# Kernel optimization log

Hardware: AMD Instinct MI355X
Metric: run time of the kernel (lower is better)

The kernel has to match this reference:

```python
import jax, jax.numpy as jnp
import numpy as np

EPS = 1e-8
BETA = 0.02          # bisector-band sharpness
ALPHA_UNION = 8.0    # exp-union strength
W_MIN, W_MAX = 0.005, 0.5
RAW_TEMP = 5.0       # width squash temperature
REL_TEMP = 0.05      # seed-relevance softmax temperature
A_MIN, A_MAX = 0.5, 2.0  # anisotropy eigenvalue range


def setup_inputs() -> dict:
    key = jax.random.key(0)
    k1, k2, k3, k4, k5 = jax.random.split(key, 5)
    N, S = 65536, 32
    return {
        "points_uv": jax.random.uniform(k1, (N, 2), dtype=jnp.float32),
        "seeds_raw": jax.random.uniform(k2, (S, 2), dtype=jnp.float32),
        "w_raw": jax.random.normal(k3, (1,), dtype=jnp.float32),
        "theta": jax.random.normal(k4, (S,), dtype=jnp.float32),
        "a_raw": jax.random.normal(k5, (S,), dtype=jnp.float32),
    }


def _metric_matrices(theta, a_raw):
    # anisotropic 2x2 SPD metrics M_s = R^T diag(a, 1/a) R
    t = jnp.tanh(a_raw)
    a = 0.5 * (A_MAX - A_MIN) * t + 0.5 * (A_MAX + A_MIN)  # (S,)
    c, s = jnp.cos(theta), jnp.sin(theta)
    R = jnp.stack([jnp.stack([c, -s], -1), jnp.stack([s, c], -1)], -2)  # (S,2,2)
    dvec = jnp.stack([a, 1.0 / (a + EPS)], -1)  # (S,2)
    return jnp.einsum("ska,sk,skb->sab", R, dvec, R)  # (S,2,2)


def reference(points_uv, seeds_raw, w_raw, theta, a_raw):
    S = seeds_raw.shape[0]
    # half-thickness around the Voronoi bisector
    w = W_MIN + (W_MAX - W_MIN) * jax.nn.sigmoid(w_raw[0] / RAW_TEMP)
    M = _metric_matrices(theta, a_raw)  # (S,2,2)

    # point-to-seed diffs with periodic wrapping on both u and v
    diff = points_uv[:, None, :] - seeds_raw[None, :, :]  # (N,S,2)
    diff = diff - jnp.round(diff)

    # anisotropic distances d_i(x) = sqrt(diff^T M_i diff)
    d = jnp.sqrt(jnp.einsum("nsa,sab,nsb->ns", diff, M, diff) + EPS)  # (N,S)

    # soft seed relevance -> soft pair weights P_ij (upper triangular, normalized)
    w_soft = jax.nn.softmax(-d / REL_TEMP, axis=1)  # (N,S)
    pair = w_soft[:, :, None] * w_soft[:, None, :]  # (N,S,S)
    mask = jnp.triu(jnp.ones((S, S), dtype=points_uv.dtype), k=1)
    pair = pair * mask
    P = pair / (pair.sum(axis=(1, 2), keepdims=True) + EPS)

    # bisector band: B_ij = sigmoid((w - |d_i - d_j|_smooth) / beta)
    Delta = d[:, :, None] - d[:, None, :]  # (N,S,S)
    abs_smooth = jnp.sqrt(Delta * Delta + EPS)
    B = jax.nn.sigmoid((w - abs_smooth) / BETA)

    # union over i<j pairs: rho = 1 - exp(-alpha * sum S_ij)
    S_sum = jnp.sum(P * B, axis=(1, 2))  # (N,)
    rho = 1.0 - jnp.exp(-ALPHA_UNION * S_sum)
    return rho
```

## Files before the change

kernel.cpp:

```cpp
#include <hip/hip_runtime.h>
#include <math.h>


#define LOG2E  1.4426950408889634f
#define EPSF   1e-8f
#define TAB_D  8192.0f
#define TAB_N  8320
#define BLOCK  512
#define PPB    64

__device__ __forceinline__ float tabB(const float* tab, unsigned a, unsigned b) {
    const unsigned hi = a > b ? a : b;
    const unsigned lo = a > b ? b : a;
    return *(const float*)((const char*)tab + (hi - lo));
}

__global__ __launch_bounds__(BLOCK) void voronoi_tab(
    const float* __restrict__ points,
    const float* __restrict__ seeds,
    const float* __restrict__ w_raw,
    const float* __restrict__ theta,
    const float* __restrict__ a_raw,
    float* __restrict__ out,
    int N, int nTiles)
{
    __shared__ float    s_tab[TAB_N];
    __shared__ unsigned s_di[PPB * 32];
    __shared__ float    s_w [PPB * 32];
    __shared__ float    s_su[32], s_sv[32], s_m00[32], s_m01[32], s_m11[32];

    const int t = threadIdx.x;

    const float wr = w_raw[0];
    const float sg = __builtin_amdgcn_rcpf(1.0f + exp2f(wr * (-LOG2E / 5.0f)));
    const float w  = 0.005f + 0.495f * sg;

    if (t < 32) {
        const float x  = a_raw[t];
        const float z  = exp2f(2.0f * LOG2E * x);
        const float th = (z - 1.0f) * __builtin_amdgcn_rcpf(z + 1.0f);
        const float a  = 0.75f * th + 1.25f;
        const float ia = __builtin_amdgcn_rcpf(a + EPSF);
        const float cs = __cosf(theta[t]);
        const float sn = __sinf(theta[t]);
        const float S2 = TAB_D * TAB_D;
        s_m00[t] = (a * cs * cs + ia * sn * sn) * S2;
        s_m01[t] = (cs * sn * (ia - a)) * S2;
        s_m11[t] = (a * sn * sn + ia * cs * cs) * S2;
        s_su[t]  = seeds[2 * t];
        s_sv[t]  = seeds[2 * t + 1];
    }

    {
        const float kC = (LOG2E / 0.02f) / TAB_D;
        const float kB = -w * (LOG2E / 0.02f);
        for (int k = t; k < TAB_N; k += BLOCK) {
            const float y = exp2f(fmaf((float)k, kC, kB));
            s_tab[k] = __builtin_amdgcn_rcpf(1.0f + y);
        }
    }
    __syncthreads();

    const int pb = t >> 3;
    const int g  = t & 7;
    const int s0 = g * 4;

    const float4 su4  = *(const float4*)&s_su[s0];
    const float4 sv4  = *(const float4*)&s_sv[s0];
    const float4 m004 = *(const float4*)&s_m00[s0];
    const float4 m014 = *(const float4*)&s_m01[s0];
    const float4 m114 = *(const float4*)&s_m11[s0];

    unsigned* dbase = &s_di[pb * 32];
    float*    wbase = &s_w [pb * 32];

    const float EPS_Q = 1e-8f * TAB_D * TAB_D;
    const float cE    = -(20.0f * LOG2E) / TAB_D;

    for (int tile = blockIdx.x; tile < nTiles; tile += gridDim.x) {
        const int p = tile * PPB + pb;
        if (p < N) {
            const float2 uv = ((const float2*)points)[p];
            const float u = uv.x, v = uv.y;

            float4 d4;
#define DIST(SU, SV, M00, M01, M11, OUTD)                                    \
            {                                                                \
                float du = u - (SU); du -= rintf(du);                        \
                float dv = v - (SV); dv -= rintf(dv);                        \
                float q = fmaf(du * du, (M00),                               \
                          fmaf(2.0f * du * dv, (M01),                       \
                          fmaf(dv * dv, (M11), EPS_Q)));                     \
                (OUTD) = sqrtf(q);                                           \
            }
            DIST(su4.x, sv4.x, m004.x, m014.x, m114.x, d4.x)
            DIST(su4.y, sv4.y, m004.y, m014.y, m114.y, d4.y)
            DIST(su4.z, sv4.z, m004.z, m014.z, m114.z, d4.z)
            DIST(su4.w, sv4.w, m004.w, m014.w, m114.w, d4.w)

            float4 e4;
            e4.x = exp2f(d4.x * cE);
            e4.y = exp2f(d4.y * cE);
            e4.z = exp2f(d4.z * cE);
            e4.w = exp2f(d4.w * cE);
            float Z = (e4.x + e4.y) + (e4.z + e4.w);
            Z += __shfl_xor(Z, 1, 64);
            Z += __shfl_xor(Z, 2, 64);
            Z += __shfl_xor(Z, 4, 64);
            const float rcpZ = __builtin_amdgcn_rcpf(Z);
            float4 w4;
            w4.x = e4.x * rcpZ; w4.y = e4.y * rcpZ;
            w4.z = e4.z * rcpZ; w4.w = e4.w * rcpZ;
            float sumsq = w4.x * w4.x;
            sumsq = fmaf(w4.y, w4.y, sumsq);
            sumsq = fmaf(w4.z, w4.z, sumsq);
            sumsq = fmaf(w4.w, w4.w, sumsq);

            uint4 ii;
            ii.x = ((unsigned)(d4.x + 0.5f)) << 2;
            ii.y = ((unsigned)(d4.y + 0.5f)) << 2;
            ii.z = ((unsigned)(d4.z + 0.5f)) << 2;
            ii.w = ((unsigned)(d4.w + 0.5f)) << 2;

            *(uint4*) (dbase + s0) = ii;
            *(float4*)(wbase + s0) = w4;

            float accb = 0.0f;
            {
                float b0 = tabB(s_tab, ii.x, ii.y) * w4.y;
                b0 = fmaf(tabB(s_tab, ii.x, ii.z), w4.z, b0);
                b0 = fmaf(tabB(s_tab, ii.x, ii.w), w4.w, b0);
                float b1 = tabB(s_tab, ii.y, ii.z) * w4.z;
                b1 = fmaf(tabB(s_tab, ii.y, ii.w), w4.w, b1);
                float b2 = tabB(s_tab, ii.z, ii.w) * w4.w;
                accb = fmaf(w4.x, b0, accb);
                accb = fmaf(w4.y, b1, accb);
                accb = fmaf(w4.z, b2, accb);
            }

#define ROT(R, ACC)                                                          \
            {                                                                \
                const int gj = ((g + (R)) & 7) * 4;                          \
                const uint4  ij = *(const uint4*) (dbase + gj);              \
                const float4 wj = *(const float4*)(wbase + gj);              \
                float b0, b1, b2, b3;                                        \
                b0 =      tabB(s_tab, ii.x, ij.x) * wj.x;                    \
                b0 = fmaf(tabB(s_tab, ii.x, ij.y), wj.y, b0);                \
                b0 = fmaf(tabB(s_tab, ii.x, ij.z), wj.z, b0);                \
                b0 = fmaf(tabB(s_tab, ii.x, ij.w), wj.w, b0);                \
                b1 =      tabB(s_tab, ii.y, ij.x) * wj.x;                    \
                b1 = fmaf(tabB(s_tab, ii.y, ij.y), wj.y, b1);                \
                b1 = fmaf(tabB(s_tab, ii.y, ij.z), wj.z, b1);                \
                b1 = fmaf(tabB(s_tab, ii.y, ij.w), wj.w, b1);                \
                b2 =      tabB(s_tab, ii.z, ij.x) * wj.x;                    \
                b2 = fmaf(tabB(s_tab, ii.z, ij.y), wj.y, b2);                \
                b2 = fmaf(tabB(s_tab, ii.z, ij.z), wj.z, b2);                \
                b2 = fmaf(tabB(s_tab, ii.z, ij.w), wj.w, b2);                \
                b3 =      tabB(s_tab, ii.w, ij.x) * wj.x;                    \
                b3 = fmaf(tabB(s_tab, ii.w, ij.y), wj.y, b3);                \
                b3 = fmaf(tabB(s_tab, ii.w, ij.z), wj.z, b3);                \
                b3 = fmaf(tabB(s_tab, ii.w, ij.w), wj.w, b3);                \
                (ACC) = fmaf(w4.x, b0, (ACC));                               \
                (ACC) = fmaf(w4.y, b1, (ACC));                               \
                (ACC) = fmaf(w4.z, b2, (ACC));                               \
                (ACC) = fmaf(w4.w, b3, (ACC));                               \
            }

            ROT(1, accb)
            ROT(2, accb)
            ROT(3, accb)
            float acc4 = 0.0f;
            ROT(4, acc4)
            accb = fmaf(0.5f, acc4, accb);

            float nb = accb, sq = sumsq;
            nb += __shfl_xor(nb, 1, 64);  sq += __shfl_xor(sq, 1, 64);
            nb += __shfl_xor(nb, 2, 64);  sq += __shfl_xor(sq, 2, 64);
            nb += __shfl_xor(nb, 4, 64);  sq += __shfl_xor(sq, 4, 64);

            const float den   = fmaxf(0.5f * (1.0f - sq), 0.0f) + EPSF;
            const float ratio = nb * __builtin_amdgcn_rcpf(den);
            const float rho   = 1.0f - exp2f(ratio * (-8.0f * LOG2E));
            if (g == 0) out[p] = rho;
        }
    }
}

extern "C" void kernel_launch(void* const* d_in, const int* in_sizes, int n_in,
                              void* d_out, int out_size, void* d_ws, size_t ws_size,
                              hipStream_t stream) {
    const float* points = (const float*)d_in[0];
    const float* seeds  = (const float*)d_in[1];
    const float* w_raw  = (const float*)d_in[2];
    const float* theta  = (const float*)d_in[3];
    const float* a_raw  = (const float*)d_in[4];
    float* out = (float*)d_out;

    const int N = in_sizes[0] / 2;
    const int nTiles = (N + PPB - 1) / PPB;
    const int grid = nTiles < 768 ? nTiles : 768;

    voronoi_tab<<<grid, BLOCK, 0, stream>>>(points, seeds, w_raw, theta, a_raw,
                                            out, N, nTiles);
}
```

Baseline: 17.57 us.

## Compute cross-group bisector sigmoids directly and shrink the signed lookup table

The 4x4 cross-group pair terms now compute the bisector sigmoid directly with exp2 and a reciprocal instead of gathering from a shared-memory table with data-dependent indices. The remaining intra-group pairs use a smaller signed-difference table with clamped indices. The persistent grid-stride loop is replaced by one 32-point tile per 256-thread block, with a higher occupancy hint. This trades scattered LDS gathers and their bank conflicts for transcendental ALU work. Every block now rebuilds its own smaller table, and there are many more blocks doing so.

```diff
diff --git a/kernel.cpp b/kernel.cpp
--- a/kernel.cpp
+++ b/kernel.cpp
@@ -4,30 +4,26 @@
 
 #define LOG2E  1.4426950408889634f
 #define EPSF   1e-8f
-#define TAB_D  8192.0f
-#define TAB_N  8320
-#define BLOCK  512
-#define PPB    64
+#define TSCALE 2048.0f
+#define TAB_N  2048
+#define TMIDB  4096
+#define BLOCK  256
+#define PPB    32
+#define SSTR   40
 
-__device__ __forceinline__ float tabB(const float* tab, unsigned a, unsigned b) {
-    const unsigned hi = a > b ? a : b;
-    const unsigned lo = a > b ? b : a;
-    return *(const float*)((const char*)tab + (hi - lo));
-}
-
-__global__ __launch_bounds__(BLOCK) void voronoi_tab(
+__global__ __launch_bounds__(BLOCK, 8) void voronoi_v4(
     const float* __restrict__ points,
     const float* __restrict__ seeds,
     const float* __restrict__ w_raw,
     const float* __restrict__ theta,
     const float* __restrict__ a_raw,
     float* __restrict__ out,
-    int N, int nTiles)
+    int N)
 {
-    __shared__ float    s_tab[TAB_N];
-    __shared__ unsigned s_di[PPB * 32];
-    __shared__ float    s_w [PPB * 32];
-    __shared__ float    s_su[32], s_sv[32], s_m00[32], s_m01[32], s_m11[32];
+    __shared__ float s_tab[TAB_N];
+    __shared__ float s_dd[PPB * SSTR];
+    __shared__ float s_ww[PPB * SSTR];
+    __shared__ float s_su[32], s_sv[32], s_m00[32], s_m01[32], s_m11[32];
 
     const int t = threadIdx.x;
 
@@ -43,19 +39,19 @@
         const float ia = __builtin_amdgcn_rcpf(a + EPSF);
         const float cs = __cosf(theta[t]);
         const float sn = __sinf(theta[t]);
-        const float S2 = TAB_D * TAB_D;
+        const float S2 = TSCALE * TSCALE;
         s_m00[t] = (a * cs * cs + ia * sn * sn) * S2;
-        s_m01[t] = (cs * sn * (ia - a)) * S2;
+        s_m01[t] = (2.0f * cs * sn * (ia - a)) * S2;
         s_m11[t] = (a * sn * sn + ia * cs * cs) * S2;
         s_su[t]  = seeds[2 * t];
         s_sv[t]  = seeds[2 * t + 1];
     }
-
     {
-        const float kC = (LOG2E / 0.02f) / TAB_D;
-        const float kB = -w * (LOG2E / 0.02f);
+        const float kC = (50.0f * LOG2E) / TSCALE;
+        const float kB = -w * (50.0f * LOG2E);
         for (int k = t; k < TAB_N; k += BLOCK) {
-            const float y = exp2f(fmaf((float)k, kC, kB));
+            const float ad = fabsf((float)(k - 1024));
+            const float y  = exp2f(fmaf(ad, kC, kB));
             s_tab[k] = __builtin_amdgcn_rcpf(1.0f + y);
         }
     }
@@ -64,6 +60,8 @@
     const int pb = t >> 3;
     const int g  = t & 7;
     const int s0 = g * 4;
+    const int p  = blockIdx.x * PPB + pb;
+    if (p >= N) return;
 
     const float4 su4  = *(const float4*)&s_su[s0];
     const float4 sv4  = *(const float4*)&s_sv[s0];
@@ -71,119 +69,114 @@
     const float4 m014 = *(const float4*)&s_m01[s0];
     const float4 m114 = *(const float4*)&s_m11[s0];
 
-    unsigned* dbase = &s_di[pb * 32];
-    float*    wbase = &s_w [pb * 32];
+    const float2 uv = ((const float2*)points)[p];
+    const float u = uv.x, v = uv.y;
 
-    const float EPS_Q = 1e-8f * TAB_D * TAB_D;
-    const float cE    = -(20.0f * LOG2E) / TAB_D;
+    const float EPS_Q = 1e-8f * TSCALE * TSCALE;
+    float4 d4;
+#define DIST(SU, SV, M00, M01, M11, OUTD)                                  \
+    {                                                                      \
+        float du = u - (SU); du -= rintf(du);                              \
+        float dv = v - (SV); dv -= rintf(dv);                              \
+        float q = fmaf(du * du, (M00),                                     \
+                  fmaf(du * dv, (M01),                                     \
+                  fmaf(dv * dv, (M11), EPS_Q)));                           \
+        (OUTD) = sqrtf(q);                                                 \
+    }
+    DIST(su4.x, sv4.x, m004.x, m014.x, m114.x, d4.x)
+    DIST(su4.y, sv4.y, m004.y, m014.y, m114.y, d4.y)
+    DIST(su4.z, sv4.z, m004.z, m014.z, m114.z, d4.z)
+    DIST(su4.w, sv4.w, m004.w, m014.w, m114.w, d4.w)
 
-    for (int tile = blockIdx.x; tile < nTiles; tile += gridDim.x) {
-        const int p = tile * PPB + pb;
-        if (p < N) {
-            const float2 uv = ((const float2*)points)[p];
-            const float u = uv.x, v = uv.y;
+    const float cE = -(20.0f * LOG2E) / TSCALE;
+    float4 e4;
+    e4.x = exp2f(d4.x * cE);
+    e4.y = exp2f(d4.y * cE);
+    e4.z = exp2f(d4.z * cE);
+    e4.w = exp2f(d4.w * cE);
+    float Z = (e4.x + e4.y) + (e4.z + e4.w);
+    Z += __shfl_xor(Z, 1, 64);
+    Z += __shfl_xor(Z, 2, 64);
+    Z += __shfl_xor(Z, 4, 64);
+    const float rcpZ = __builtin_amdgcn_rcpf(Z);
+    float4 w4;
+    w4.x = e4.x * rcpZ; w4.y = e4.y * rcpZ;
+    w4.z = e4.z * rcpZ; w4.w = e4.w * rcpZ;
+    float sumsq = w4.x * w4.x;
+    sumsq = fmaf(w4.y, w4.y, sumsq);
+    sumsq = fmaf(w4.z, w4.z, sumsq);
+    sumsq = fmaf(w4.w, w4.w, sumsq);
 
-            float4 d4;
-#define DIST(SU, SV, M00, M01, M11, OUTD)                                    \
-            {                                                                \
-                float du = u - (SU); du -= rintf(du);                        \
-                float dv = v - (SV); dv -= rintf(dv);                        \
-                float q = fmaf(du * du, (M00),                               \
-                          fmaf(2.0f * du * dv, (M01),                       \
-                          fmaf(dv * dv, (M11), EPS_Q)));                     \
-                (OUTD) = sqrtf(q);                                           \
-            }
-            DIST(su4.x, sv4.x, m004.x, m014.x, m114.x, d4.x)
-            DIST(su4.y, sv4.y, m004.y, m014.y, m114.y, d4.y)
-            DIST(su4.z, sv4.z, m004.z, m014.z, m114.z, d4.z)
-            DIST(su4.w, sv4.w, m004.w, m014.w, m114.w, d4.w)
+    float* db = &s_dd[pb * SSTR];
+    float* wb = &s_ww[pb * SSTR];
+    *(float4*)(db + s0) = d4;
+    *(float4*)(wb + s0) = w4;
 
-            float4 e4;
-            e4.x = exp2f(d4.x * cE);
-            e4.y = exp2f(d4.y * cE);
-            e4.z = exp2f(d4.z * cE);
-            e4.w = exp2f(d4.w * cE);
-            float Z = (e4.x + e4.y) + (e4.z + e4.w);
-            Z += __shfl_xor(Z, 1, 64);
-            Z += __shfl_xor(Z, 2, 64);
-            Z += __shfl_xor(Z, 4, 64);
-            const float rcpZ = __builtin_amdgcn_rcpf(Z);
-            float4 w4;
-            w4.x = e4.x * rcpZ; w4.y = e4.y * rcpZ;
-            w4.z = e4.z * rcpZ; w4.w = e4.w * rcpZ;
-            float sumsq = w4.x * w4.x;
-            sumsq = fmaf(w4.y, w4.y, sumsq);
-            sumsq = fmaf(w4.z, w4.z, sumsq);
-            sumsq = fmaf(w4.w, w4.w, sumsq);
+    const char* tb = (const char*)s_tab;
+    int K = (int)(TSCALE * w) + 370;
+    if (K > 1023) K = 1023;
+    const int lo = TMIDB - 4 * K, hi = TMIDB + 4 * K;
+#define TBODY(DI, DJ, WJ, ACC)                                             \
+    {                                                                      \
+        int off = (int)fmaf((DI) - (DJ), 4.0f, (float)(TMIDB + 2));        \
+        off = off < lo ? lo : (off > hi ? hi : off);                       \
+        off &= ~3;                                                         \
+        const float B = *(const float*)(tb + off);                         \
+        (ACC) = fmaf((WJ), B, (ACC));                                      \
+    }
+    float b0, b1, b2, b3;
+    b0 = 0.0f; b1 = 0.0f; b2 = 0.0f; b3 = 0.0f;
+    TBODY(d4.x, d4.y, w4.y, b0)
+    TBODY(d4.x, d4.z, w4.z, b0)
+    TBODY(d4.x, d4.w, w4.w, b0)
+    TBODY(d4.y, d4.z, w4.z, b1)
+    TBODY(d4.y, d4.w, w4.w, b1)
+    TBODY(d4.z, d4.w, w4.w, b2)
 
-            uint4 ii;
-            ii.x = ((unsigned)(d4.x + 0.5f)) << 2;
-            ii.y = ((unsigned)(d4.y + 0.5f)) << 2;
-            ii.z = ((unsigned)(d4.z + 0.5f)) << 2;
-            ii.w = ((unsigned)(d4.w + 0.5f)) << 2;
+    const float C1 = (50.0f * LOG2E) / TSCALE;
+    const float C0 = -w * (50.0f * LOG2E);
+#define EBODY(DI, DJ, WJ, ACC)                                             \
+    {                                                                      \
+        const float ex = exp2f(fmaf(fabsf((DI) - (DJ)), C1, C0));          \
+        const float B  = __builtin_amdgcn_rcpf(1.0f + ex);                 \
+        (ACC) = fmaf((WJ), B, (ACC));                                      \
+    }
+#define ROTE(R, HALF)                                                      \
+    {                                                                      \
+        const int gj = ((g + (R)) & 7) * 4;                                \
+        const float4 dj = *(const float4*)(db + gj);                       \
+        float4 wj = *(const float4*)(wb + gj);                             \
+        if (HALF) {                                                        \
+            wj.x *= 0.5f; wj.y *= 0.5f; wj.z *= 0.5f; wj.w *= 0.5f;        \
+        }                                                                  \
+        EBODY(d4.x, dj.x, wj.x, b0) EBODY(d4.x, dj.y, wj.y, b0)            \
+        EBODY(d4.x, dj.z, wj.z, b0) EBODY(d4.x, dj.w, wj.w, b0)            \
+        EBODY(d4.y, dj.x, wj.x, b1) EBODY(d4.y, dj.y, wj.y, b1)            \
+        EBODY(d4.y, dj.z, wj.z, b1) EBODY(d4.y, dj.w, wj.w, b1)            \
+        EBODY(d4.z, dj.x, wj.x, b2) EBODY(d4.z, dj.y, wj.y, b2)            \
+        EBODY(d4.z, dj.z, wj.z, b2) EBODY(d4.z, dj.w, wj.w, b2)            \
+        EBODY(d4.w, dj.x, wj.x, b3) EBODY(d4.w, dj.y, wj.y, b3)            \
+        EBODY(d4.w, dj.z, wj.z, b3) EBODY(d4.w, dj.w, wj.w, b3)            \
+    }
+    ROTE(1, 0)
+    ROTE(2, 0)
+    ROTE(3, 0)
+    ROTE(4, 1)
 
-            *(uint4*) (dbase + s0) = ii;
-            *(float4*)(wbase + s0) = w4;
+    float accb = w4.x * b0;
+    accb = fmaf(w4.y, b1, accb);
+    accb = fmaf(w4.z, b2, accb);
+    accb = fmaf(w4.w, b3, accb);
 
-            float accb = 0.0f;
-            {
-                float b0 = tabB(s_tab, ii.x, ii.y) * w4.y;
-                b0 = fmaf(tabB(s_tab, ii.x, ii.z), w4.z, b0);
-                b0 = fmaf(tabB(s_tab, ii.x, ii.w), w4.w, b0);
-                float b1 = tabB(s_tab, ii.y, ii.z) * w4.z;
-                b1 = fmaf(tabB(s_tab, ii.y, ii.w), w4.w, b1);
-                float b2 = tabB(s_tab, ii.z, ii.w) * w4.w;
-                accb = fmaf(w4.x, b0, accb);
-                accb = fmaf(w4.y, b1, accb);
-                accb = fmaf(w4.z, b2, accb);
-            }
+    float nb = accb, sq = sumsq;
+    nb += __shfl_xor(nb, 1, 64);  sq += __shfl_xor(sq, 1, 64);
+    nb += __shfl_xor(nb, 2, 64);  sq += __shfl_xor(sq, 2, 64);
+    nb += __shfl_xor(nb, 4, 64);  sq += __shfl_xor(sq, 4, 64);
 
-#define ROT(R, ACC)                                                          \
-            {                                                                \
-                const int gj = ((g + (R)) & 7) * 4;                          \
-                const uint4  ij = *(const uint4*) (dbase + gj);              \
-                const float4 wj = *(const float4*)(wbase + gj);              \
-                float b0, b1, b2, b3;                                        \
-                b0 =      tabB(s_tab, ii.x, ij.x) * wj.x;                    \
-                b0 = fmaf(tabB(s_tab, ii.x, ij.y), wj.y, b0);                \
-                b0 = fmaf(tabB(s_tab, ii.x, ij.z), wj.z, b0);                \
-                b0 = fmaf(tabB(s_tab, ii.x, ij.w), wj.w, b0);                \
-                b1 =      tabB(s_tab, ii.y, ij.x) * wj.x;                    \
-                b1 = fmaf(tabB(s_tab, ii.y, ij.y), wj.y, b1);                \
-                b1 = fmaf(tabB(s_tab, ii.y, ij.z), wj.z, b1);                \
-                b1 = fmaf(tabB(s_tab, ii.y, ij.w), wj.w, b1);                \
-                b2 =      tabB(s_tab, ii.z, ij.x) * wj.x;                    \
-                b2 = fmaf(tabB(s_tab, ii.z, ij.y), wj.y, b2);                \
-                b2 = fmaf(tabB(s_tab, ii.z, ij.z), wj.z, b2);                \
-                b2 = fmaf(tabB(s_tab, ii.z, ij.w), wj.w, b2);                \
-                b3 =      tabB(s_tab, ii.w, ij.x) * wj.x;                    \
-                b3 = fmaf(tabB(s_tab, ii.w, ij.y), wj.y, b3);                \
-                b3 = fmaf(tabB(s_tab, ii.w, ij.z), wj.z, b3);                \
-                b3 = fmaf(tabB(s_tab, ii.w, ij.w), wj.w, b3);                \
-                (ACC) = fmaf(w4.x, b0, (ACC));                               \
-                (ACC) = fmaf(w4.y, b1, (ACC));                               \
-                (ACC) = fmaf(w4.z, b2, (ACC));                               \
-                (ACC) = fmaf(w4.w, b3, (ACC));                               \
-            }
-
-            ROT(1, accb)
-            ROT(2, accb)
-            ROT(3, accb)
-            float acc4 = 0.0f;
-            ROT(4, acc4)
-            accb = fmaf(0.5f, acc4, accb);
-
-            float nb = accb, sq = sumsq;
-            nb += __shfl_xor(nb, 1, 64);  sq += __shfl_xor(sq, 1, 64);
-            nb += __shfl_xor(nb, 2, 64);  sq += __shfl_xor(sq, 2, 64);
-            nb += __shfl_xor(nb, 4, 64);  sq += __shfl_xor(sq, 4, 64);
-
-            const float den   = fmaxf(0.5f * (1.0f - sq), 0.0f) + EPSF;
-            const float ratio = nb * __builtin_amdgcn_rcpf(den);
-            const float rho   = 1.0f - exp2f(ratio * (-8.0f * LOG2E));
-            if (g == 0) out[p] = rho;
-        }
-    }
+    const float den   = fmaxf(0.5f * (1.0f - sq), 0.0f) + EPSF;
+    const float ratio = nb * __builtin_amdgcn_rcpf(den);
+    const float rho   = 1.0f - exp2f(ratio * (-8.0f * LOG2E));
+    if (g == 0) out[p] = rho;
 }
 
 extern "C" void kernel_launch(void* const* d_in, const int* in_sizes, int n_in,
@@ -197,9 +190,8 @@
     float* out = (float*)d_out;
 
     const int N = in_sizes[0] / 2;
-    const int nTiles = (N + PPB - 1) / PPB;
-    const int grid = nTiles < 768 ? nTiles : 768;
+    const int grid = (N + PPB - 1) / PPB;
 
-    voronoi_tab<<<grid, BLOCK, 0, stream>>>(points, seeds, w_raw, theta, a_raw,
-                                            out, N, nTiles);
+    voronoi_v4<<<grid, BLOCK, 0, stream>>>(points, seeds, w_raw, theta, a_raw,
+                                           out, N);
 }
```

New measurement: 23.01 us. 1.31x slower.
